# Kernel tuning notes

Hardware: AMD Instinct MI355X
Metric: run time of the kernel (lower is better)

## Reference

```python
import jax, jax.numpy as jnp
import numpy as np

H = 4      # num_heads
DH = 32    # head dim (hidden_size // num_heads)


def _seg_softmax(logits, seg, n):
    # numerically stable segment softmax over axis 0, segments of size n
    m = jax.ops.segment_max(logits, seg, num_segments=n)
    e = jnp.exp(logits - m[seg])
    s = jax.ops.segment_sum(e, seg, num_segments=n)
    return e / (s[seg] + 1e-16)


def setup_inputs() -> dict:
    key = jax.random.key(0)
    ks = jax.random.split(key, 16)
    N, E, EE, C = 50000, 400000, 800000, 800000
    NIN, EIN, HID, EMB = 1, 32, 128, 32
    inp = {
        'x': jax.random.normal(ks[0], (N, NIN), jnp.float32),
        'edge_index': jax.random.randint(ks[1], (2, E), 0, N),
        'edge_attr': jax.random.normal(ks[2], (E, EIN), jnp.float32),
        'edge_to_edge_index': jax.random.randint(ks[3], (2, EE), 0, E),
        'node_to_node_index': jax.random.randint(ks[4], (2, C), 0, N),
        'W1': jax.random.normal(ks[5], (2 * NIN + EIN, EMB), jnp.float32) / np.sqrt(2 * NIN + EIN),
        'b1': jnp.zeros((EMB,), jnp.float32),
        'W2': jax.random.normal(ks[6], (EMB, HID), jnp.float32) / np.sqrt(EMB),
        'b2': jnp.zeros((HID,), jnp.float32),
        'Wq': jax.random.normal(ks[7], (HID, HID), jnp.float32) / np.sqrt(HID),
        'Wk': jax.random.normal(ks[8], (HID, HID), jnp.float32) / np.sqrt(HID),
        'Wv': jax.random.normal(ks[9], (HID, HID), jnp.float32) / np.sqrt(HID),
        'Wq2': jax.random.normal(ks[10], (1, HID), jnp.float32),
        'Wk2': jax.random.normal(ks[11], (1, HID), jnp.float32),
        'Wv2': jax.random.normal(ks[12], (1, HID), jnp.float32),
    }
    return inp


def reference(x, edge_index, edge_attr, edge_to_edge_index, node_to_node_index,
              W1, b1, W2, b2, Wq, Wk, Wv, Wq2, Wk2, Wv2):
    N = x.shape[0]
    E = edge_attr.shape[0]
    # --- NodeToEdgeAggregation: gather endpoint node feats, concat edge attr, MLP ---
    s, d = edge_index[0], edge_index[1]
    h = jnp.concatenate([x[s], x[d], edge_attr], axis=-1)          # [E, 2*nin+ein]
    h = jax.nn.relu(h @ W1 + b1) @ W2 + b2                          # [E, hidden]
    # --- EdgeToEdgeAggregation: multi-head attention on the line graph ---
    es, ed = edge_to_edge_index[0], edge_to_edge_index[1]
    q = (h @ Wq)[ed].reshape(-1, H, DH)                             # [EE, H, DH]
    k = (h @ Wk)[es].reshape(-1, H, DH)
    v = (h @ Wv)[es].reshape(-1, H, DH)
    logits = (q * k).sum(-1) / jnp.sqrt(jnp.float32(DH))            # [EE, H]
    alpha = _seg_softmax(logits, ed, E)                             # softmax over incoming edge-neighbors
    agg_e = jax.ops.segment_sum(alpha[..., None] * v, ed, num_segments=E)  # [E, H, DH]
    updated_edge_feat = agg_e.reshape(E, -1).mean(axis=1, keepdims=True)   # [E, 1]
    # --- EdgeToNodeAggregation over combined node+edge feature array ---
    nef = jnp.concatenate([x, updated_edge_feat], axis=0)           # [N+E, 1]
    ns, nd = node_to_node_index[0], node_to_node_index[1]
    q2 = (nef[nd] @ Wq2).reshape(-1, H, DH)                         # [C, H, DH]
    k2 = (nef[ns] @ Wk2).reshape(-1, H, DH)
    v2 = (nef[ns] @ Wv2).reshape(-1, H, DH)
    logits2 = (q2 * k2).sum(-1) / jnp.sqrt(jnp.float32(DH))         # [C, H]
    alpha2 = _seg_softmax(logits2, nd, N + E)
    msgs = (alpha2[..., None] * v2).reshape(ns.shape[0], -1).mean(axis=1)  # [C]
    aggregated_node_feat = jax.ops.segment_sum(msgs, nd, num_segments=N)   # [N]
    return (aggregated_node_feat, updated_edge_feat)
```

## Files before the change

kernel.cpp:

```cpp
#include <hip/hip_runtime.h>
#include <stdint.h>

#define HIDN 128
#define EMBN 32
#define PCAP 16
#define NCAP 64
#define PSEGSH 10
#define NSEGSH 7
#define PSEG (1 << PSEGSH)
#define NSEG (1 << NSEGSH)
#define PBCAP 2816
#define NBCAP 2816
#define CHUNK 2048
#define MAXBINS 400

typedef __attribute__((ext_vector_type(8))) short bf16x8;
typedef __attribute__((ext_vector_type(4))) float f32x4;
typedef unsigned long long u64;

__device__ __forceinline__ unsigned bf16r(float f) {
  unsigned u = __float_as_uint(f);
  return (u + 0x7FFFu + ((u >> 16) & 1u)) >> 16;
}
__device__ __forceinline__ unsigned pack2(float a, float b) {
  return bf16r(a) | (bf16r(b) << 16);
}
__device__ __forceinline__ float blo(unsigned u) { return __uint_as_float(u << 16); }
__device__ __forceinline__ float bhi(unsigned u) { return __uint_as_float(u & 0xFFFF0000u); }
__device__ __forceinline__ float4 f4fma(float s, float4 a, float4 b) {
  return make_float4(fmaf(s, a.x, b.x), fmaf(s, a.y, b.y), fmaf(s, a.z, b.z), fmaf(s, a.w, b.w));
}
__device__ __forceinline__ float4 f4max0(float4 a) {
  return make_float4(fmaxf(a.x, 0.f), fmaxf(a.y, 0.f), fmaxf(a.z, 0.f), fmaxf(a.w, 0.f));
}

__global__ __launch_bounds__(256) void k_prep1(
    const float* __restrict__ W2, const float* __restrict__ b2,
    const float* __restrict__ Wq, const float* __restrict__ Wk, const float* __restrict__ Wv,
    float* __restrict__ Wqp, float* __restrict__ Wkp, float* __restrict__ bqp,
    float* __restrict__ Wvsp, float* __restrict__ bvs)
{
  __shared__ float swvs[HIDN * 4];
  int t = threadIdx.x;
  if (blockIdx.x == 33) {
    for (int idx = t; idx < HIDN * 4; idx += 256) {
      int l = idx >> 2, h = idx & 3;
      float s = 0.f;
      const float* wl = Wv + l * HIDN + h * 32;
      for (int dh = 0; dh < 32; dh++) s += wl[dh];
      swvs[idx] = s;
    }
    __syncthreads();
    if (t < 128) {
      int i = t >> 2, h = t & 3;
      float a = 0.f;
      for (int l = 0; l < HIDN; l++) a = fmaf(W2[i * HIDN + l], swvs[l * 4 + h], a);
      Wvsp[t] = a;
    } else if (t < 132) {
      int h = t - 128;
      float a = 0.f;
      for (int l = 0; l < HIDN; l++) a = fmaf(b2[l], swvs[l * 4 + h], a);
      bvs[h] = a;
    }
    return;
  }
  int idx = blockIdx.x * 256 + t;
  if (idx < 8192) {
    int q = idx < 4096;
    int tt = q ? idx : idx - 4096;
    int i = tt >> 7, j = tt & 127;
    const float* W = q ? Wq : Wk;
    float a = 0.f;
    for (int l = 0; l < HIDN; l++)
      a = fmaf(W2[i * HIDN + l], W[l * HIDN + j], a);
    (q ? Wqp : Wkp)[tt] = a;
  } else if (idx < 8320) {
    int j = idx - 8192;
    float a = 0.f;
    for (int l = 0; l < HIDN; l++)
      a = fmaf(b2[l], Wq[l * HIDN + j], a);
    bqp[j] = a;
  }
}

__global__ __launch_bounds__(256, 4) void k_front(
    const float* __restrict__ x, const int* __restrict__ eidx, const float* __restrict__ ea,
    const float* __restrict__ W1, const float* __restrict__ b1,
    const float* __restrict__ Wvsp, const float* __restrict__ bvs,
    unsigned* __restrict__ embB, uint2* __restrict__ vsb,
    const int* __restrict__ e2e, int* __restrict__ goffP, u64* __restrict__ partP,
    const int* __restrict__ n2n, int* __restrict__ goffN, u64* __restrict__ partN,
    int E, int EE, int C, int N, int nEdgeB, int nPartP, int PBINS, int NBINS)
{
  __shared__ int lcnt[MAXBINS];
  __shared__ int lbase[MAXBINS];
  int b = blockIdx.x;
  int tid = threadIdx.x;
  if (b < nEdgeB) {
    int e = b * 256 + tid;
    if (e >= E) return;
    int si = eidx[e], di = eidx[E + e];
    float xs = x[si], xd = x[di];

    const float4* b4  = (const float4*)b1;
    const float4* w0  = (const float4*)W1;
    const float4* w1r = (const float4*)(W1 + 32);
    float4 E0, E1, E2, E3, E4, E5, E6, E7;
#define INIT(i) E##i = f4fma(xs, w0[i], f4fma(xd, w1r[i], b4[i]));
    INIT(0) INIT(1) INIT(2) INIT(3) INIT(4) INIT(5) INIT(6) INIT(7)
#undef INIT
    const float4* ea4 = (const float4*)(ea + (size_t)e * 32);
#define ROW(c, wr) { const float4* w_ = (const float4*)(W1 + (size_t)(wr) * 32); \
  E0 = f4fma(c, w_[0], E0); E1 = f4fma(c, w_[1], E1); E2 = f4fma(c, w_[2], E2); E3 = f4fma(c, w_[3], E3); \
  E4 = f4fma(c, w_[4], E4); E5 = f4fma(c, w_[5], E5); E6 = f4fma(c, w_[6], E6); E7 = f4fma(c, w_[7], E7); }
#pragma unroll
    for (int rb = 0; rb < 8; rb++) {
      float4 v = ea4[rb];
      ROW(v.x, 2 + rb * 4 + 0)
      ROW(v.y, 2 + rb * 4 + 1)
      ROW(v.z, 2 + rb * 4 + 2)
      ROW(v.w, 2 + rb * 4 + 3)
    }
#undef ROW
    E0 = f4max0(E0); E1 = f4max0(E1); E2 = f4max0(E2); E3 = f4max0(E3);
    E4 = f4max0(E4); E5 = f4max0(E5); E6 = f4max0(E6); E7 = f4max0(E7);

    uint4 p0, p1, p2, p3;
    p0.x = pack2(E0.x, E0.y); p0.y = pack2(E0.z, E0.w); p0.z = pack2(E1.x, E1.y); p0.w = pack2(E1.z, E1.w);
    p1.x = pack2(E2.x, E2.y); p1.y = pack2(E2.z, E2.w); p1.z = pack2(E3.x, E3.y); p1.w = pack2(E3.z, E3.w);
    p2.x = pack2(E4.x, E4.y); p2.y = pack2(E4.z, E4.w); p2.z = pack2(E5.x, E5.y); p2.w = pack2(E5.z, E5.w);
    p3.x = pack2(E6.x, E6.y); p3.y = pack2(E6.z, E6.w); p3.z = pack2(E7.x, E7.y); p3.w = pack2(E7.z, E7.w);
    uint4* er = (uint4*)(embB + (size_t)e * 16);
    er[0] = p0; er[1] = p1; er[2] = p2; er[3] = p3;

    const float4* wv = (const float4*)Wvsp;
    float4 vs = *(const float4*)bvs;
#define VK(k) { vs = f4fma(E##k.x, wv[4*k+0], vs); vs = f4fma(E##k.y, wv[4*k+1], vs); \
                vs = f4fma(E##k.z, wv[4*k+2], vs); vs = f4fma(E##k.w, wv[4*k+3], vs); }
    VK(0) VK(1) VK(2) VK(3) VK(4) VK(5) VK(6) VK(7)
#undef VK
    vsb[e] = make_uint2(pack2(vs.x, vs.y), pack2(vs.z, vs.w));
  } else if (b < nEdgeB + nPartP) {
    int start = (b - nEdgeB) * CHUNK;
    for (int i = tid; i < PBINS; i += 256) lcnt[i] = 0;
    __syncthreads();
#pragma unroll 4
    for (int k = 0; k < 8; k++) {
      int p = start + k * 256 + tid;
      if (p < EE) atomicAdd(&lcnt[e2e[EE + p] >> PSEGSH], 1);
    }
    __syncthreads();
    for (int i = tid; i < PBINS; i += 256) {
      int c = lcnt[i];
      lbase[i] = c ? atomicAdd(&goffP[i], c) : 0;
      lcnt[i] = 0;
    }
    __syncthreads();
#pragma unroll 4
    for (int k = 0; k < 8; k++) {
      int p = start + k * 256 + tid;
      if (p < EE) {
        int es = e2e[p], ed = e2e[EE + p];
        int bin = ed >> PSEGSH;
        int pos = atomicAdd(&lcnt[bin], 1) + lbase[bin];
        if (pos < PBCAP)
          partP[(size_t)bin * PBCAP + pos] = ((u64)(unsigned)ed << 32) | (unsigned)es;
      }
    }
  } else {
    int start = (b - nEdgeB - nPartP) * CHUNK;
    for (int i = tid; i < NBINS; i += 256) lcnt[i] = 0;
    __syncthreads();
#pragma unroll 4
    for (int k = 0; k < 8; k++) {
      int c = start + k * 256 + tid;
      if (c < C) {
        int nd = n2n[C + c];
        if (nd < N) atomicAdd(&lcnt[nd >> NSEGSH], 1);
      }
    }
    __syncthreads();
    for (int i = tid; i < NBINS; i += 256) {
      int c = lcnt[i];
      lbase[i] = c ? atomicAdd(&goffN[i], c) : 0;
      lcnt[i] = 0;
    }
    __syncthreads();
#pragma unroll 4
    for (int k = 0; k < 8; k++) {
      int c = start + k * 256 + tid;
      if (c < C) {
        int ns = n2n[c], nd = n2n[C + c];
        if (nd < N) {
          int bin = nd >> NSEGSH;
          unsigned pay = __float_as_uint(x[ns]);
          int pos = atomicAdd(&lcnt[bin], 1) + lbase[bin];
          if (pos < NBCAP)
            partN[(size_t)bin * NBCAP + pos] = ((u64)(unsigned)nd << 32) | pay;
        }
      }
    }
  }
}

__global__ __launch_bounds__(256) void k_fill(
    const int* __restrict__ goffP, const u64* __restrict__ partP,
    int* __restrict__ pcnt, int* __restrict__ pbucket,
    const float* __restrict__ Wqp, const float* __restrict__ Wkp,
    const float* __restrict__ bqp,
    const float* __restrict__ Wq2, const float* __restrict__ Wk2, const float* __restrict__ Wv2,
    unsigned short* __restrict__ MBpk, float* __restrict__ c2th,
    float* __restrict__ dhd, float* __restrict__ wv2s,
    int E, int PBINS)
{
  extern __shared__ int lds[];
  const float rs = 0.17677669529663687f;
  int b = blockIdx.x;
  int tid = threadIdx.x;
  if (b < PBINS) {
    int seg0 = b << PSEGSH;
    int nseg = E - seg0; if (nseg > PSEG) nseg = PSEG;
    int* cnt = lds;
    int* rows = lds + PSEG;
    for (int i = tid; i < nseg; i += 256) cnt[i] = 0;
    __syncthreads();
    int g = goffP[b]; if (g > PBCAP) g = PBCAP;
    for (int i = tid; i < g; i += 256) {
      u64 pk = partP[(size_t)b * PBCAP + i];
      int ed = (int)(pk >> 32);
      int es = (int)(unsigned)pk;
      int s = ed - seg0;
      int pos = atomicAdd(&cnt[s], 1);
      if (pos < PCAP) rows[s * PCAP + pos] = es;
    }
    __syncthreads();
    for (int i = tid; i < nseg; i += 256) pcnt[seg0 + i] = cnt[i];
    int tot = nseg * PCAP;
    for (int i = tid; i < tot; i += 256)
      pbucket[(size_t)seg0 * PCAP + i] = rows[i];
  } else {
    int idx = (b - PBINS) * 256 + tid;
    if (idx < 4096) {
      int jj = idx & 7, lane = (idx >> 3) & 63, nb = (idx >> 9) & 1, h = idx >> 10;
      int k = (lane >> 4) * 8 + jj;
      int n = nb * 16 + (lane & 15);
      float a = 0.f;
      const float* wq = Wqp + k * HIDN + h * 32;
      const float* wk = Wkp + n * HIDN + h * 32;
      for (int j = 0; j < 32; j++) a = fmaf(wq[j], wk[j], a);
      MBpk[idx] = (unsigned short)bf16r(a * rs);
    } else if (idx < 4224) {
      int t = idx - 4096;
      int h = t >> 5, ip = t & 31;
      float a2 = 0.f;
      for (int j = 0; j < 32; j++)
        a2 = fmaf(bqp[h * 32 + j], Wkp[ip * HIDN + h * 32 + j], a2);
      c2th[h * 32 + ip] = a2 * rs;
    } else if (idx < 4228) {
      int h = idx - 4224;
      float d = 0.f, wsum = 0.f;
      for (int dh = 0; dh < 32; dh++) {
        d = fmaf(Wq2[h * 32 + dh], Wk2[h * 32 + dh], d);
        wsum += Wv2[h * 32 + dh];
      }
      dhd[h]  = d * rs;
      wv2s[h] = wsum;
    }
  }
}

__global__ __launch_bounds__(256, 4) void k_back(
    const unsigned* __restrict__ embB, const unsigned short* __restrict__ MBpk,
    const uint2* __restrict__ vsb, const float* __restrict__ c2th,
    const int* __restrict__ pcnt, const int* __restrict__ pbucket,
    const int* __restrict__ goffN, const u64* __restrict__ partN,
    const float* __restrict__ x, const float* __restrict__ dhd, const float* __restrict__ wv2s,
    float* __restrict__ out0, float* __restrict__ out1,
    int E, int N, int NBINS)
{
  __shared__ float qtl[256 * 33];
  int b = blockIdx.x;
  int tid = threadIdx.x;
  if (b < NBINS) {
    int seg0 = b << NSEGSH;
    int nseg = N - seg0; if (nseg > NSEG) nseg = NSEG;
    int* cnt = (int*)qtl;
    float* rows = qtl + NSEG;
    for (int i = tid; i < nseg; i += 256) cnt[i] = 0;
    __syncthreads();
    int g = goffN[b]; if (g > NBCAP) g = NBCAP;
    for (int i = tid; i < g; i += 256) {
      u64 pk = partN[(size_t)b * NBCAP + i];
      int nd = (int)(pk >> 32);
      int s = nd - seg0;
      int pos = atomicAdd(&cnt[s], 1);
      if (pos < NCAP) rows[s * NCAP + pos] = __uint_as_float((unsigned)pk);
    }
    __syncthreads();
    for (int t = tid; t < nseg * 4; t += 256) {
      int s = t >> 2, h = t & 3;
      int c = cnt[s]; c = c < NCAP ? c : NCAP;
      int nd = seg0 + s;
      float xn = x[nd];
      float d = dhd[h];
      const float* bkt = rows + s * NCAP;

      float amx = -3.4e38f, amn = 3.4e38f;
      for (int n = 0; n < c; n++) {
        float a = xn * bkt[n];
        amx = fmaxf(amx, a); amn = fminf(amn, a);
      }
      float m = (d > 0.f) ? d * amx : d * amn;

      float den = 0.f, num = 0.f;
      for (int n = 0; n < c; n++) {
        float asv = bkt[n];
        float ev = __expf(fmaf(xn * asv, d, -m));
        den += ev;
        num = fmaf(ev, asv, num);
      }
      float r = wv2s[h] * num / (den + 1e-16f);
      r += __shfl_xor(r, 1);
      r += __shfl_xor(r, 2);
      if (h == 0) out0[nd] = r * 0.0078125f;
    }
  } else {
    int pb = b - NBINS;
    int wave = tid >> 6, lane = tid & 63;
    int e0 = pb * 64;
    int we0 = e0 + wave * 16;

    union { uint4 u; bf16x8 bv; } af;
    af.u = *((const uint4*)(embB + ((size_t)(we0 + (lane & 15)) << 4)) + (lane >> 4));

#pragma unroll
    for (int h = 0; h < 4; h++) {
#pragma unroll
      for (int nb = 0; nb < 2; nb++) {
        union { uint4 u; bf16x8 bv; } bf;
        bf.u = *(const uint4*)(MBpk + (((h * 2 + nb) * 64 + lane) << 3));
        int col = nb * 16 + (lane & 15);
        float c2v = c2th[h * 32 + col];
        f32x4 acc = {c2v, c2v, c2v, c2v};
        acc = __builtin_amdgcn_mfma_f32_16x16x32_bf16(af.bv, bf.bv, acc, 0, 0, 0);
        int rowb = wave * 16 + (lane >> 4) * 4;
#pragma unroll
        for (int r = 0; r < 4; r++)
          qtl[((rowb + r) * 4 + h) * 33 + col] = acc[r];
      }
    }
    __syncthreads();

    int e = e0 + (tid >> 2);
    if (e >= E) return;
    int h = tid & 3;
    const float* q = qtl + tid * 33;

    int cnt = pcnt[e];
    cnt = cnt < PCAP ? cnt : PCAP;
    float den = 0.f, num = 0.f;
    for (int n = 0; n < cnt; n++) {
      int es = pbucket[(size_t)e * PCAP + n];
      const uint4* ep = (const uint4*)(embB + ((size_t)es << 4));
      uint4 u0 = ep[0], u1 = ep[1], u2 = ep[2], u3 = ep[3];
      uint2 vu = vsb[es];
      unsigned vh = (h & 2) ? vu.y : vu.x;
      float vsv = (h & 1) ? bhi(vh) : blo(vh);
      float dot = 0.f;
#define DOT8(uu, base) \
      dot = fmaf(q[base + 0], blo(uu.x), dot); dot = fmaf(q[base + 1], bhi(uu.x), dot); \
      dot = fmaf(q[base + 2], blo(uu.y), dot); dot = fmaf(q[base + 3], bhi(uu.y), dot); \
      dot = fmaf(q[base + 4], blo(uu.z), dot); dot = fmaf(q[base + 5], bhi(uu.z), dot); \
      dot = fmaf(q[base + 6], blo(uu.w), dot); dot = fmaf(q[base + 7], bhi(uu.w), dot);
      DOT8(u0, 0) DOT8(u1, 8) DOT8(u2, 16) DOT8(u3, 24)
#undef DOT8
      float ex = __expf(dot);
      den += ex;
      num = fmaf(ex, vsv, num);
    }
    float r = num / (den + 1e-16f);
    r += __shfl_xor(r, 1);
    r += __shfl_xor(r, 2);
    if (h == 0) out1[e] = r * 0.0078125f;
  }
}

extern "C" void kernel_launch(void* const* d_in, const int* in_sizes, int n_in,
                              void* d_out, int out_size, void* d_ws, size_t ws_size,
                              hipStream_t stream)
{
  const float* x   = (const float*)d_in[0];
  const int*   eidx= (const int*)d_in[1];
  const float* ea  = (const float*)d_in[2];
  const int*   e2e = (const int*)d_in[3];
  const int*   n2n = (const int*)d_in[4];
  const float* W1  = (const float*)d_in[5];
  const float* b1  = (const float*)d_in[6];
  const float* W2  = (const float*)d_in[7];
  const float* b2  = (const float*)d_in[8];
  const float* Wq  = (const float*)d_in[9];
  const float* Wk  = (const float*)d_in[10];
  const float* Wv  = (const float*)d_in[11];
  const float* Wq2 = (const float*)d_in[12];
  const float* Wk2 = (const float*)d_in[13];
  const float* Wv2 = (const float*)d_in[14];

  const int N  = in_sizes[0];
  const int E  = in_sizes[1] / 2;
  const int EE = in_sizes[3] / 2;
  const int C  = in_sizes[4] / 2;

  float* out0 = (float*)d_out;
  float* out1 = (float*)d_out + N;

  const int PBINS = (E + PSEG - 1) >> PSEGSH;
  const int NBINS = (N + NSEG - 1) >> NSEGSH;

  char* w = (char*)d_ws;
  size_t off = 0;
  auto alloc = [&](size_t bytes) -> char* {
    char* p = w + off;
    off += (bytes + 255) & ~(size_t)255;
    return p;
  };
  float* Wqp   = (float*)alloc(EMBN * HIDN * 4);
  float* Wkp   = (float*)alloc(EMBN * HIDN * 4);
  float* bqp   = (float*)alloc(HIDN * 4);
  unsigned short* MBpk = (unsigned short*)alloc(4096 * 2);
  float* c2th  = (float*)alloc(4 * EMBN * 4);
  float* Wvsp  = (float*)alloc(EMBN * 4 * 4);
  float* bvs   = (float*)alloc(16);
  float* dhd   = (float*)alloc(16);
  float* wv2s  = (float*)alloc(16);
  unsigned* embB = (unsigned*)alloc((size_t)E * 16 * 4);
  uint2* vsb   = (uint2*)alloc((size_t)E * 8);
  u64*   partP = (u64*)alloc((size_t)PBINS * PBCAP * 8);
  u64*   partN = (u64*)alloc((size_t)NBINS * NBCAP * 8);
  int*   pbucket = (int*)alloc((size_t)E * PCAP * 4);
  int*   pcnt  = (int*)alloc((size_t)E * 4);
  char* zbase = w + off;
  int*   goffP = (int*)alloc((size_t)PBINS * 4);
  int*   goffN = (int*)alloc((size_t)NBINS * 4);
  size_t zbytes = (size_t)((w + off) - zbase);

  const int nEdgeB = (E + 255) / 256;
  const int nPartP = (EE + CHUNK - 1) / CHUNK;
  const int nPartN = (C + CHUNK - 1) / CHUNK;
  const int nPairMfmaB = (E + 63) / 64;
  const int nPrep2B = 17;
  const size_t fillLDS = (size_t)(PSEG + PSEG * PCAP) * 4;

  hipMemsetAsync(zbase, 0, zbytes, stream);

  k_prep1<<<34, 256, 0, stream>>>(W2, b2, Wq, Wk, Wv, Wqp, Wkp, bqp, Wvsp, bvs);
  k_front<<<nEdgeB + nPartP + nPartN, 256, 0, stream>>>(
      x, eidx, ea, W1, b1, Wvsp, bvs, embB, vsb,
      e2e, goffP, partP, n2n, goffN, partN,
      E, EE, C, N, nEdgeB, nPartP, PBINS, NBINS);
  k_fill<<<PBINS + nPrep2B, 256, fillLDS, stream>>>(
      goffP, partP, pcnt, pbucket,
      Wqp, Wkp, bqp, Wq2, Wk2, Wv2, MBpk, c2th, dhd, wv2s, E, PBINS);
  k_back<<<NBINS + nPairMfmaB, 256, 0, stream>>>(
      embB, MBpk, vsb, c2th, pcnt, pbucket, goffN, partN,
      x, dhd, wv2s, out0, out1, E, N, NBINS);
}
```

Baseline: 232.8 us.

## Fuse bucket fill into attention kernel and cache partition ranks in registers

Removes the separate k_fill kernel. Each k_back block now builds its per-edge neighbor buckets in LDS from the partitioned pairs and consumes them directly, so pbucket/pcnt no longer take a global round trip. The prep2 weight work moves into k_front as extra blocks. The partition passes keep loaded indices and their LDS atomic ranks in registers instead of reloading and recounting, and bins shrink to 512 edges to fit the larger LDS footprint. The costs are much higher LDS use per k_back block (about 66KB) and lower occupancy, and the MFMA query computation becomes a serial loop inside each bin with extra syncs.

```diff
diff --git a/kernel.cpp b/kernel.cpp
--- a/kernel.cpp
+++ b/kernel.cpp
@@ -5,14 +5,14 @@
 #define EMBN 32
 #define PCAP 16
 #define NCAP 64
-#define PSEGSH 10
+#define PSEGSH 9
 #define NSEGSH 7
 #define PSEG (1 << PSEGSH)
 #define NSEG (1 << NSEGSH)
-#define PBCAP 2816
+#define PBCAP 1536
 #define NBCAP 2816
 #define CHUNK 2048
-#define MAXBINS 400
+#define MAXBINS 800
 
 typedef __attribute__((ext_vector_type(8))) short bf16x8;
 typedef __attribute__((ext_vector_type(4))) float f32x4;
@@ -83,17 +83,22 @@
   }
 }
 
-__global__ __launch_bounds__(256, 4) void k_front(
+__global__ __launch_bounds__(256, 6) void k_front(
     const float* __restrict__ x, const int* __restrict__ eidx, const float* __restrict__ ea,
     const float* __restrict__ W1, const float* __restrict__ b1,
     const float* __restrict__ Wvsp, const float* __restrict__ bvs,
     unsigned* __restrict__ embB, uint2* __restrict__ vsb,
     const int* __restrict__ e2e, int* __restrict__ goffP, u64* __restrict__ partP,
     const int* __restrict__ n2n, int* __restrict__ goffN, u64* __restrict__ partN,
-    int E, int EE, int C, int N, int nEdgeB, int nPartP, int PBINS, int NBINS)
+    const float* __restrict__ Wqp, const float* __restrict__ Wkp, const float* __restrict__ bqp,
+    const float* __restrict__ Wq2, const float* __restrict__ Wk2, const float* __restrict__ Wv2,
+    unsigned short* __restrict__ MBpk, float* __restrict__ c2th,
+    float* __restrict__ dhd, float* __restrict__ wv2s,
+    int E, int EE, int C, int N, int nEdgeB, int nPartP, int nPartN, int PBINS, int NBINS)
 {
   __shared__ int lcnt[MAXBINS];
   __shared__ int lbase[MAXBINS];
+  const float rs = 0.17677669529663687f;
   int b = blockIdx.x;
   int tid = threadIdx.x;
   if (b < nEdgeB) {
@@ -144,102 +149,65 @@
     int start = (b - nEdgeB) * CHUNK;
     for (int i = tid; i < PBINS; i += 256) lcnt[i] = 0;
     __syncthreads();
-#pragma unroll 4
+    int rankv[8], esv[8], edv[8];
+#pragma unroll
     for (int k = 0; k < 8; k++) {
       int p = start + k * 256 + tid;
-      if (p < EE) atomicAdd(&lcnt[e2e[EE + p] >> PSEGSH], 1);
+      rankv[k] = -1;
+      if (p < EE) {
+        esv[k] = e2e[p];
+        edv[k] = e2e[EE + p];
+        rankv[k] = atomicAdd(&lcnt[edv[k] >> PSEGSH], 1);
+      }
     }
     __syncthreads();
     for (int i = tid; i < PBINS; i += 256) {
       int c = lcnt[i];
       lbase[i] = c ? atomicAdd(&goffP[i], c) : 0;
-      lcnt[i] = 0;
-    }
-    __syncthreads();
-#pragma unroll 4
+    }
+    __syncthreads();
+#pragma unroll
     for (int k = 0; k < 8; k++) {
-      int p = start + k * 256 + tid;
-      if (p < EE) {
-        int es = e2e[p], ed = e2e[EE + p];
-        int bin = ed >> PSEGSH;
-        int pos = atomicAdd(&lcnt[bin], 1) + lbase[bin];
+      if (rankv[k] >= 0) {
+        int bin = edv[k] >> PSEGSH;
+        int pos = rankv[k] + lbase[bin];
         if (pos < PBCAP)
-          partP[(size_t)bin * PBCAP + pos] = ((u64)(unsigned)ed << 32) | (unsigned)es;
-      }
-    }
-  } else {
+          partP[(size_t)bin * PBCAP + pos] = ((u64)(unsigned)edv[k] << 32) | (unsigned)esv[k];
+      }
+    }
+  } else if (b < nEdgeB + nPartP + nPartN) {
     int start = (b - nEdgeB - nPartP) * CHUNK;
     for (int i = tid; i < NBINS; i += 256) lcnt[i] = 0;
     __syncthreads();
-#pragma unroll 4
+    int rankv[8], nsv[8], ndv[8];
+#pragma unroll
     for (int k = 0; k < 8; k++) {
       int c = start + k * 256 + tid;
+      rankv[k] = -1;
       if (c < C) {
-        int nd = n2n[C + c];
-        if (nd < N) atomicAdd(&lcnt[nd >> NSEGSH], 1);
+        nsv[k] = n2n[c];
+        ndv[k] = n2n[C + c];
+        if (ndv[k] < N) rankv[k] = atomicAdd(&lcnt[ndv[k] >> NSEGSH], 1);
       }
     }
     __syncthreads();
     for (int i = tid; i < NBINS; i += 256) {
       int c = lcnt[i];
       lbase[i] = c ? atomicAdd(&goffN[i], c) : 0;
-      lcnt[i] = 0;
-    }
-    __syncthreads();
-#pragma unroll 4
+    }
+    __syncthreads();
+#pragma unroll
     for (int k = 0; k < 8; k++) {
-      int c = start + k * 256 + tid;
-      if (c < C) {
-        int ns = n2n[c], nd = n2n[C + c];
-        if (nd < N) {
-          int bin = nd >> NSEGSH;
-          unsigned pay = __float_as_uint(x[ns]);
-          int pos = atomicAdd(&lcnt[bin], 1) + lbase[bin];
-          if (pos < NBCAP)
-            partN[(size_t)bin * NBCAP + pos] = ((u64)(unsigned)nd << 32) | pay;
-        }
-      }
-    }
-  }
-}
-
-__global__ __launch_bounds__(256) void k_fill(
-    const int* __restrict__ goffP, const u64* __restrict__ partP,
-    int* __restrict__ pcnt, int* __restrict__ pbucket,
-    const float* __restrict__ Wqp, const float* __restrict__ Wkp,
-    const float* __restrict__ bqp,
-    const float* __restrict__ Wq2, const float* __restrict__ Wk2, const float* __restrict__ Wv2,
-    unsigned short* __restrict__ MBpk, float* __restrict__ c2th,
-    float* __restrict__ dhd, float* __restrict__ wv2s,
-    int E, int PBINS)
-{
-  extern __shared__ int lds[];
-  const float rs = 0.17677669529663687f;
-  int b = blockIdx.x;
-  int tid = threadIdx.x;
-  if (b < PBINS) {
-    int seg0 = b << PSEGSH;
-    int nseg = E - seg0; if (nseg > PSEG) nseg = PSEG;
-    int* cnt = lds;
-    int* rows = lds + PSEG;
-    for (int i = tid; i < nseg; i += 256) cnt[i] = 0;
-    __syncthreads();
-    int g = goffP[b]; if (g > PBCAP) g = PBCAP;
-    for (int i = tid; i < g; i += 256) {
-      u64 pk = partP[(size_t)b * PBCAP + i];
-      int ed = (int)(pk >> 32);
-      int es = (int)(unsigned)pk;
-      int s = ed - seg0;
-      int pos = atomicAdd(&cnt[s], 1);
-      if (pos < PCAP) rows[s * PCAP + pos] = es;
-    }
-    __syncthreads();
-    for (int i = tid; i < nseg; i += 256) pcnt[seg0 + i] = cnt[i];
-    int tot = nseg * PCAP;
-    for (int i = tid; i < tot; i += 256)
-      pbucket[(size_t)seg0 * PCAP + i] = rows[i];
+      if (rankv[k] >= 0) {
+        int bin = ndv[k] >> NSEGSH;
+        int pos = rankv[k] + lbase[bin];
+        if (pos < NBCAP)
+          partN[(size_t)bin * NBCAP + pos] =
+              ((u64)(unsigned)ndv[k] << 32) | __float_as_uint(x[nsv[k]]);
+      }
+    }
   } else {
-    int idx = (b - PBINS) * 256 + tid;
+    int idx = (b - nEdgeB - nPartP - nPartN) * 256 + tid;
     if (idx < 4096) {
       int jj = idx & 7, lane = (idx >> 3) & 63, nb = (idx >> 9) & 1, h = idx >> 10;
       int k = (lane >> 4) * 8 + jj;
@@ -269,37 +237,39 @@
   }
 }
 
-__global__ __launch_bounds__(256, 4) void k_back(
+__global__ __launch_bounds__(256, 2) void k_back(
     const unsigned* __restrict__ embB, const unsigned short* __restrict__ MBpk,
     const uint2* __restrict__ vsb, const float* __restrict__ c2th,
-    const int* __restrict__ pcnt, const int* __restrict__ pbucket,
+    const int* __restrict__ goffP, const u64* __restrict__ partP,
     const int* __restrict__ goffN, const u64* __restrict__ partN,
     const float* __restrict__ x, const float* __restrict__ dhd, const float* __restrict__ wv2s,
     float* __restrict__ out0, float* __restrict__ out1,
     int E, int N, int NBINS)
 {
-  __shared__ float qtl[256 * 33];
+  extern __shared__ char smem[];
+  float* qtl = (float*)smem;
+  int* cntl  = (int*)(smem + 33792);
+  int* rowsl = cntl + 512;
   int b = blockIdx.x;
   int tid = threadIdx.x;
   if (b < NBINS) {
     int seg0 = b << NSEGSH;
     int nseg = N - seg0; if (nseg > NSEG) nseg = NSEG;
-    int* cnt = (int*)qtl;
-    float* rows = qtl + NSEG;
-    for (int i = tid; i < nseg; i += 256) cnt[i] = 0;
+    float* rows = (float*)rowsl;
+    for (int i = tid; i < nseg; i += 256) cntl[i] = 0;
     __syncthreads();
     int g = goffN[b]; if (g > NBCAP) g = NBCAP;
     for (int i = tid; i < g; i += 256) {
       u64 pk = partN[(size_t)b * NBCAP + i];
       int nd = (int)(pk >> 32);
       int s = nd - seg0;
-      int pos = atomicAdd(&cnt[s], 1);
+      int pos = atomicAdd(&cntl[s], 1);
       if (pos < NCAP) rows[s * NCAP + pos] = __uint_as_float((unsigned)pk);
     }
     __syncthreads();
     for (int t = tid; t < nseg * 4; t += 256) {
       int s = t >> 2, h = t & 3;
-      int c = cnt[s]; c = c < NCAP ? c : NCAP;
+      int c = cntl[s]; c = c < NCAP ? c : NCAP;
       int nd = seg0 + s;
       float xn = x[nd];
       float d = dhd[h];
@@ -326,62 +296,79 @@
     }
   } else {
     int pb = b - NBINS;
+    int seg0 = pb << PSEGSH;
+    int nseg = E - seg0; if (nseg > PSEG) nseg = PSEG;
     int wave = tid >> 6, lane = tid & 63;
-    int e0 = pb * 64;
-    int we0 = e0 + wave * 16;
-
-    union { uint4 u; bf16x8 bv; } af;
-    af.u = *((const uint4*)(embB + ((size_t)(we0 + (lane & 15)) << 4)) + (lane >> 4));
-
-#pragma unroll
-    for (int h = 0; h < 4; h++) {
-#pragma unroll
-      for (int nb = 0; nb < 2; nb++) {
-        union { uint4 u; bf16x8 bv; } bf;
-        bf.u = *(const uint4*)(MBpk + (((h * 2 + nb) * 64 + lane) << 3));
-        int col = nb * 16 + (lane & 15);
-        float c2v = c2th[h * 32 + col];
-        f32x4 acc = {c2v, c2v, c2v, c2v};
-        acc = __builtin_amdgcn_mfma_f32_16x16x32_bf16(af.bv, bf.bv, acc, 0, 0, 0);
-        int rowb = wave * 16 + (lane >> 4) * 4;
-#pragma unroll
-        for (int r = 0; r < 4; r++)
-          qtl[((rowb + r) * 4 + h) * 33 + col] = acc[r];
-      }
-    }
-    __syncthreads();
-
-    int e = e0 + (tid >> 2);
-    if (e >= E) return;
-    int h = tid & 3;
-    const float* q = qtl + tid * 33;
-
-    int cnt = pcnt[e];
-    cnt = cnt < PCAP ? cnt : PCAP;
-    float den = 0.f, num = 0.f;
-    for (int n = 0; n < cnt; n++) {
-      int es = pbucket[(size_t)e * PCAP + n];
-      const uint4* ep = (const uint4*)(embB + ((size_t)es << 4));
-      uint4 u0 = ep[0], u1 = ep[1], u2 = ep[2], u3 = ep[3];
-      uint2 vu = vsb[es];
-      unsigned vh = (h & 2) ? vu.y : vu.x;
-      float vsv = (h & 1) ? bhi(vh) : blo(vh);
-      float dot = 0.f;
+    for (int i = tid; i < nseg; i += 256) cntl[i] = 0;
+    __syncthreads();
+    int g = goffP[pb]; if (g > PBCAP) g = PBCAP;
+    for (int i = tid; i < g; i += 256) {
+      u64 pk = partP[(size_t)pb * PBCAP + i];
+      int ed = (int)(pk >> 32);
+      int es = (int)(unsigned)pk;
+      int s = ed - seg0;
+      int pos = atomicAdd(&cntl[s], 1);
+      if (pos < PCAP) rowsl[s * PCAP + pos] = es;
+    }
+    __syncthreads();
+
+    for (int t0 = 0; t0 < nseg; t0 += 64) {
+      int we0 = seg0 + t0 + wave * 16;
+      union { uint4 u; bf16x8 bv; } af;
+      af.u = *((const uint4*)(embB + ((size_t)(we0 + (lane & 15)) << 4)) + (lane >> 4));
+#pragma unroll
+      for (int h = 0; h < 4; h++) {
+#pragma unroll
+        for (int nb = 0; nb < 2; nb++) {
+          union { uint4 u; bf16x8 bv; } bf;
+          bf.u = *(const uint4*)(MBpk + (((h * 2 + nb) * 64 + lane) << 3));
+          int col = nb * 16 + (lane & 15);
+          float c2v = c2th[h * 32 + col];
+          f32x4 acc = {c2v, c2v, c2v, c2v};
+          acc = __builtin_amdgcn_mfma_f32_16x16x32_bf16(af.bv, bf.bv, acc, 0, 0, 0);
+          int rowb = wave * 16 + (lane >> 4) * 4;
+#pragma unroll
+          for (int r = 0; r < 4; r++)
+            qtl[((rowb + r) * 4 + h) * 33 + col] = acc[r];
+        }
+      }
+      __syncthreads();
+
+      int el = t0 + (tid >> 2);
+      int e = seg0 + el;
+      if (e < E) {
+        int h = tid & 3;
+        const float* q = qtl + ((tid & 255) - (t0 << 2)) * 33 + 0;
+        q = qtl + tid * 33;
+        int cnt = cntl[el];
+        cnt = cnt < PCAP ? cnt : PCAP;
+        float den = 0.f, num = 0.f;
+        for (int n = 0; n < cnt; n++) {
+          int es = rowsl[el * PCAP + n];
+          const uint4* ep = (const uint4*)(embB + ((size_t)es << 4));
+          uint4 u0 = ep[0], u1 = ep[1], u2 = ep[2], u3 = ep[3];
+          uint2 vu = vsb[es];
+          unsigned vh = (h & 2) ? vu.y : vu.x;
+          float vsv = (h & 1) ? bhi(vh) : blo(vh);
+          float dot = 0.f;
 #define DOT8(uu, base) \
-      dot = fmaf(q[base + 0], blo(uu.x), dot); dot = fmaf(q[base + 1], bhi(uu.x), dot); \
-      dot = fmaf(q[base + 2], blo(uu.y), dot); dot = fmaf(q[base + 3], bhi(uu.y), dot); \
-      dot = fmaf(q[base + 4], blo(uu.z), dot); dot = fmaf(q[base + 5], bhi(uu.z), dot); \
-      dot = fmaf(q[base + 6], blo(uu.w), dot); dot = fmaf(q[base + 7], bhi(uu.w), dot);
-      DOT8(u0, 0) DOT8(u1, 8) DOT8(u2, 16) DOT8(u3, 24)
+          dot = fmaf(q[base + 0], blo(uu.x), dot); dot = fmaf(q[base + 1], bhi(uu.x), dot); \
+          dot = fmaf(q[base + 2], blo(uu.y), dot); dot = fmaf(q[base + 3], bhi(uu.y), dot); \
+          dot = fmaf(q[base + 4], blo(uu.z), dot); dot = fmaf(q[base + 5], bhi(uu.z), dot); \
+          dot = fmaf(q[base + 6], blo(uu.w), dot); dot = fmaf(q[base + 7], bhi(uu.w), dot);
+          DOT8(u0, 0) DOT8(u1, 8) DOT8(u2, 16) DOT8(u3, 24)
 #undef DOT8
-      float ex = __expf(dot);
-      den += ex;
-      num = fmaf(ex, vsv, num);
-    }
-    float r = num / (den + 1e-16f);
-    r += __shfl_xor(r, 1);
-    r += __shfl_xor(r, 2);
-    if (h == 0) out1[e] = r * 0.0078125f;
+          float ex = __expf(dot);
+          den += ex;
+          num = fmaf(ex, vsv, num);
+        }
+        float r = num / (den + 1e-16f);
+        r += __shfl_xor(r, 1);
+        r += __shfl_xor(r, 2);
+        if (h == 0) out1[e] = r * 0.0078125f;
+      }
+      __syncthreads();
+    }
   }
 }
 
@@ -436,8 +423,6 @@
   uint2* vsb   = (uint2*)alloc((size_t)E * 8);
   u64*   partP = (u64*)alloc((size_t)PBINS * PBCAP * 8);
   u64*   partN = (u64*)alloc((size_t)NBINS * NBCAP * 8);
-  int*   pbucket = (int*)alloc((size_t)E * PCAP * 4);
-  int*   pcnt  = (int*)alloc((size_t)E * 4);
   char* zbase = w + off;
   int*   goffP = (int*)alloc((size_t)PBINS * 4);
   int*   goffN = (int*)alloc((size_t)NBINS * 4);
@@ -446,21 +431,18 @@
   const int nEdgeB = (E + 255) / 256;
   const int nPartP = (EE + CHUNK - 1) / CHUNK;
   const int nPartN = (C + CHUNK - 1) / CHUNK;
-  const int nPairMfmaB = (E + 63) / 64;
   const int nPrep2B = 17;
-  const size_t fillLDS = (size_t)(PSEG + PSEG * PCAP) * 4;
+  const size_t backLDS = 33792 + 512 * 4 + 512 * PCAP * 4;
 
   hipMemsetAsync(zbase, 0, zbytes, stream);
 
   k_prep1<<<34, 256, 0, stream>>>(W2, b2, Wq, Wk, Wv, Wqp, Wkp, bqp, Wvsp, bvs);
-  k_front<<<nEdgeB + nPartP + nPartN, 256, 0, stream>>>(
+  k_front<<<nEdgeB + nPartP + nPartN + nPrep2B, 256, 0, stream>>>(
       x, eidx, ea, W1, b1, Wvsp, bvs, embB, vsb,
       e2e, goffP, partP, n2n, goffN, partN,
-      E, EE, C, N, nEdgeB, nPartP, PBINS, NBINS);
-  k_fill<<<PBINS + nPrep2B, 256, fillLDS, stream>>>(
-      goffP, partP, pcnt, pbucket,
-      Wqp, Wkp, bqp, Wq2, Wk2, Wv2, MBpk, c2th, dhd, wv2s, E, PBINS);
-  k_back<<<NBINS + nPairMfmaB, 256, 0, stream>>>(
-      embB, MBpk, vsb, c2th, pcnt, pbucket, goffN, partN,
+      Wqp, Wkp, bqp, Wq2, Wk2, Wv2, MBpk, c2th, dhd, wv2s,
+      E, EE, C, N, nEdgeB, nPartP, nPartN, PBINS, NBINS);
+  k_back<<<NBINS + PBINS, 256, backLDS, stream>>>(
+      embB, MBpk, vsb, c2th, goffP, partP, goffN, partN,
       x, dhd, wv2s, out0, out1, E, N, NBINS);
 }
```

Result: slower. 241.6 us (+3.8%).
